# Optimization experiments

Hardware: AMD Instinct MI355X
Metric: run time of the kernel (lower is better)

## Reference

```python
import jax, jax.numpy as jnp
import numpy as np

MASK_VALUE = -1000000.0  # matches torch sequence_mask fill value


def setup_inputs() -> dict:
    key = jax.random.key(0)
    k1, k2, k3, k4 = jax.random.split(key, 4)
    B, Tq, Tk, d = 16, 2048, 2048, 128
    queries = jax.random.normal(k1, (B, Tq, d), dtype=jnp.float32)
    keys = jax.random.normal(k2, (B, Tk, d), dtype=jnp.float32)
    values = jax.random.normal(k3, (B, Tk, d), dtype=jnp.float32)
    valid_lens = jax.random.randint(k4, (B, Tq), 0, Tk, dtype=jnp.int64)
    return {"queries": queries, "keys": keys, "values": values,
            "valid_lens": valid_lens}


def reference(queries, keys, values, valid_lens):
    d = queries.shape[-1]
    Tk = keys.shape[1]
    # scores: [B, Tq, Tk]
    scores = jnp.einsum('bqd,bkd->bqk', queries, keys) / jnp.sqrt(
        jnp.asarray(d, dtype=queries.dtype))
    # per-row length mask: position k is valid iff k < valid_lens[b, q]
    mask = jnp.arange(Tk)[None, None, :] < valid_lens[:, :, None]
    scores = jnp.where(mask, scores, jnp.asarray(MASK_VALUE, scores.dtype))
    attn = jax.nn.softmax(scores, axis=-1)
    # dropout p=0.0 -> identity
    return jnp.einsum('bqk,bkd->bqd', attn, values)
```

## Files before the change

### kernel.cpp

```cpp
#include <hip/hip_runtime.h>
#include <stdint.h>
#include <math.h>

#define NB 16
#define TQ 2048
#define TK 2048
#define DH 128
#define KT (TK / 64)

#define QK_STR 136
#define VT_STR 72
#define P_STR  72

typedef __attribute__((ext_vector_type(8))) short bf16x8;
typedef __attribute__((ext_vector_type(4))) float f32x4;
typedef __attribute__((ext_vector_type(8))) unsigned short u16x8;

__device__ __forceinline__ unsigned short f2b(float f) {
  union { float f; uint32_t u; } v; v.f = f;
  uint32_t u = v.u;
  return (unsigned short)((u + 0x7fffu + ((u >> 16) & 1u)) >> 16);
}

__device__ __forceinline__ u16x8 cvt8(const float* p) {
  const f32x4 a = *(const f32x4*)p;
  const f32x4 b = *(const f32x4*)(p + 4);
  u16x8 o;
#pragma unroll
  for (int j = 0; j < 4; ++j) { o[j] = f2b(a[j]); o[4 + j] = f2b(b[j]); }
  return o;
}

__global__ __launch_bounds__(256) void prep_kernel(const float* __restrict__ K,
                                                   const float* __restrict__ V,
                                                   unsigned short* __restrict__ Kb,
                                                   unsigned short* __restrict__ Vt) {
  __shared__ alignas(16) unsigned short tile[64][136];
  const int t = threadIdx.x;
  const int b = blockIdx.y;
  const int kt = blockIdx.x;
  const int k0 = kt * 64;

  const float* Ks = K + ((size_t)b * TK + k0) * DH;
  unsigned short* Kd = Kb + ((size_t)b * TK + k0) * DH;
#pragma unroll
  for (int i = 0; i < 4; ++i) {
    const int row = i * 16 + (t >> 4);
    const int c0 = (t & 15) * 8;
    *(u16x8*)(Kd + (size_t)row * DH + c0) = cvt8(Ks + (size_t)row * DH + c0);
  }
  const float* Vs = V + ((size_t)b * TK + k0) * DH;
#pragma unroll
  for (int i = 0; i < 4; ++i) {
    const int row = i * 16 + (t >> 4);
    const int c0 = (t & 15) * 8;
    *(u16x8*)(&tile[row][c0]) = cvt8(Vs + (size_t)row * DH + c0);
  }
  __syncthreads();
  {
    const int d = t >> 1;
    const int half = t & 1;
    alignas(16) unsigned short tmp[32];
#pragma unroll
    for (int j = 0; j < 32; ++j) tmp[j] = tile[half * 32 + j][d];
    unsigned short* dst = Vt + ((size_t)(b * KT + kt) * DH + d) * 64 + half * 32;
#pragma unroll
    for (int j = 0; j < 4; ++j)
      *(u16x8*)(dst + j * 8) = *(const u16x8*)(&tmp[j * 8]);
  }
}

__global__ __launch_bounds__(256) void attn_ws(const float* __restrict__ Q,
                                               const unsigned short* __restrict__ Kp,
                                               const unsigned short* __restrict__ Vp,
                                               const int* __restrict__ vlen,
                                               float* __restrict__ out) {
  __shared__ alignas(16) char smem[53248];
  __shared__ int s_bvl[4];
  unsigned short* sQ = (unsigned short*)smem;
  unsigned short* sK = (unsigned short*)(smem + 17408);
  unsigned short* sV = (unsigned short*)(smem + 34816);

  const int tid  = threadIdx.x;
  const int w    = tid >> 6;
  const int lane = tid & 63;
  const int quad = lane >> 4;
  const int l15  = lane & 15;
  const int b    = blockIdx.y;
  const int q0   = blockIdx.x * 64;

  const float* Qb = Q + ((size_t)b * TQ + q0) * DH;
#pragma unroll
  for (int i = 0; i < 4; ++i) {
    const int row = i * 16 + (tid >> 4);
    const int c0 = (tid & 15) * 8;
    *(u16x8*)(sQ + row * QK_STR + c0) = cvt8(Qb + (size_t)row * DH + c0);
  }

  int hw = 0;
#pragma unroll
  for (int i = 0; i < 8; ++i) hw |= vlen[2 * i + 1];
  const bool is64 = (hw == 0);

  const float kScaleL2 = 0.08838834764831845f * 1.4426950408889634f;
  const float kBias    = -32.0f;
  const float kKill    = -1.0e7f;

  const int qw = q0 + w * 16;
  int vlr[4];
  float scl[4];
#pragma unroll
  for (int r = 0; r < 4; ++r) {
    const int idx = b * TQ + qw + quad * 4 + r;
    int v = is64 ? vlen[2 * idx] : vlen[idx];
    v = (v < 0) ? 0 : ((v > TK) ? TK : v);
    scl[r] = (v == 0) ? 0.0f : kScaleL2;
    vlr[r] = (v == 0) ? TK : v;
  }
  int wvl = 0;
#pragma unroll
  for (int r = 0; r < 4; ++r) wvl = max(wvl, vlr[r]);
  wvl = max(wvl, __shfl_xor(wvl, 16, 64));
  wvl = max(wvl, __shfl_xor(wvl, 32, 64));
  if (lane == 0) s_bvl[w] = wvl;

  __syncthreads();
  const int bvl = max(max(s_bvl[0], s_bvl[1]), max(s_bvl[2], s_bvl[3]));
  const int nt = (bvl + 63) >> 6;

  bf16x8 qa[4];
  {
    const unsigned short* qrow = sQ + (w * 16 + l15) * QK_STR;
#pragma unroll
    for (int kc = 0; kc < 4; ++kc)
      qa[kc] = *(const bf16x8*)(qrow + (kc * 4 + quad) * 8);
  }
  unsigned short* sP = (unsigned short*)smem + w * (16 * P_STR);

  f32x4 Of[8] = {};
  float l_r[4] = {0.f, 0.f, 0.f, 0.f};

  const unsigned short* Kbase = Kp + (size_t)b * TK * DH;
  const unsigned short* Vbase = Vp + (size_t)(b * KT) * DH * 64;
  const int krow = tid >> 4;
  const int kch  = tid & 15;

  u16x8 kreg[4], vreg[4];
  {
#pragma unroll
    for (int i = 0; i < 4; ++i)
      kreg[i] = *(const u16x8*)(Kbase + (size_t)(i * 16 + krow) * DH + kch * 8);
#pragma unroll
    for (int i = 0; i < 4; ++i)
      vreg[i] = *(const u16x8*)(Vbase + (i * 256 + tid) * 8);
  }

  for (int t = 0; t < nt; ++t) {
#pragma unroll
    for (int i = 0; i < 4; ++i)
      *(u16x8*)(sK + (i * 16 + krow) * QK_STR + kch * 8) = kreg[i];
#pragma unroll
    for (int i = 0; i < 4; ++i) {
      const int chunk = i * 256 + tid;
      *(u16x8*)(sV + (chunk >> 3) * VT_STR + (chunk & 7) * 8) = vreg[i];
    }
    __syncthreads();

    if (t + 1 < nt) {
      const unsigned short* Ksrc = Kbase + (size_t)(t + 1) * 64 * DH;
#pragma unroll
      for (int i = 0; i < 4; ++i)
        kreg[i] = *(const u16x8*)(Ksrc + (size_t)(i * 16 + krow) * DH + kch * 8);
      const unsigned short* Vsrc = Vbase + (size_t)(t + 1) * (DH * 64);
#pragma unroll
      for (int i = 0; i < 4; ++i)
        vreg[i] = *(const u16x8*)(Vsrc + (i * 256 + tid) * 8);
    }

    const int k0 = t * 64;
    if (k0 < wvl) {
      f32x4 sc[4] = {};
#pragma unroll
      for (int ct = 0; ct < 4; ++ct) {
        const unsigned short* kr = sK + (ct * 16 + l15) * QK_STR;
#pragma unroll
        for (int kc = 0; kc < 4; ++kc) {
          const bf16x8 kf = *(const bf16x8*)(kr + (kc * 4 + quad) * 8);
          sc[ct] = __builtin_amdgcn_mfma_f32_16x16x32_bf16(qa[kc], kf, sc[ct], 0, 0, 0);
        }
      }

      unsigned short pb[4][4];
#pragma unroll
      for (int ct = 0; ct < 4; ++ct) {
        const int kpos = k0 + ct * 16 + l15;
#pragma unroll
        for (int r = 0; r < 4; ++r) {
          const float s = (kpos < vlr[r]) ? fmaf(sc[ct][r], scl[r], kBias) : kKill;
          const float p = exp2f(s);
          l_r[r] += p;
          pb[ct][r] = f2b(p);
        }
      }

#pragma unroll
      for (int ct = 0; ct < 4; ++ct)
#pragma unroll
        for (int r = 0; r < 4; ++r)
          sP[(quad * 4 + r) * P_STR + ct * 16 + l15] = pb[ct][r];
      __asm__ __volatile__("" ::: "memory");

      bf16x8 pa[2];
      {
        const unsigned short* pr = sP + l15 * P_STR;
#pragma unroll
        for (int ch = 0; ch < 2; ++ch)
          pa[ch] = *(const bf16x8*)(pr + (ch * 4 + quad) * 8);
      }

#pragma unroll
      for (int dt = 0; dt < 8; ++dt) {
        const unsigned short* vr = sV + (dt * 16 + l15) * VT_STR;
#pragma unroll
        for (int ch = 0; ch < 2; ++ch) {
          const bf16x8 vf = *(const bf16x8*)(vr + (ch * 4 + quad) * 8);
          Of[dt] = __builtin_amdgcn_mfma_f32_16x16x32_bf16(pa[ch], vf, Of[dt], 0, 0, 0);
        }
      }
    }
    __syncthreads();
  }

#pragma unroll
  for (int off = 1; off <= 8; off <<= 1)
#pragma unroll
    for (int r = 0; r < 4; ++r)
      l_r[r] += __shfl_xor(l_r[r], off, 64);

#pragma unroll
  for (int r = 0; r < 4; ++r) {
    const float inv = 1.0f / l_r[r];
    const int q = qw + quad * 4 + r;
    float* orow = out + ((size_t)b * TQ + q) * DH;
#pragma unroll
    for (int dt = 0; dt < 8; ++dt)
      orow[dt * 16 + l15] = Of[dt][r] * inv;
  }
}

__global__ __launch_bounds__(256) void attn_fb(const float* __restrict__ Q,
                                               const float* __restrict__ Kp,
                                               const float* __restrict__ Vp,
                                               const int* __restrict__ vlen,
                                               float* __restrict__ out) {
  __shared__ alignas(16) char smem[53248];
  __shared__ int s_bvl[4];
  unsigned short* sQ = (unsigned short*)smem;
  unsigned short* sK = (unsigned short*)(smem + 17408);
  unsigned short* sV = (unsigned short*)(smem + 34816);

  const int tid  = threadIdx.x;
  const int w    = tid >> 6;
  const int lane = tid & 63;
  const int quad = lane >> 4;
  const int l15  = lane & 15;
  const int b    = blockIdx.y;
  const int q0   = blockIdx.x * 64;

  const float* Qb = Q + ((size_t)b * TQ + q0) * DH;
#pragma unroll
  for (int i = 0; i < 4; ++i) {
    const int row = i * 16 + (tid >> 4);
    const int c0 = (tid & 15) * 8;
    *(u16x8*)(sQ + row * QK_STR + c0) = cvt8(Qb + (size_t)row * DH + c0);
  }

  int hw = 0;
#pragma unroll
  for (int i = 0; i < 8; ++i) hw |= vlen[2 * i + 1];
  const bool is64 = (hw == 0);

  const float kScaleL2 = 0.08838834764831845f * 1.4426950408889634f;
  const float kBias    = -32.0f;
  const float kKill    = -1.0e7f;

  const int qw = q0 + w * 16;
  int vlr[4];
  float scl[4];
#pragma unroll
  for (int r = 0; r < 4; ++r) {
    const int idx = b * TQ + qw + quad * 4 + r;
    int v = is64 ? vlen[2 * idx] : vlen[idx];
    v = (v < 0) ? 0 : ((v > TK) ? TK : v);
    scl[r] = (v == 0) ? 0.0f : kScaleL2;
    vlr[r] = (v == 0) ? TK : v;
  }
  int wvl = 0;
#pragma unroll
  for (int r = 0; r < 4; ++r) wvl = max(wvl, vlr[r]);
  wvl = max(wvl, __shfl_xor(wvl, 16, 64));
  wvl = max(wvl, __shfl_xor(wvl, 32, 64));
  if (lane == 0) s_bvl[w] = wvl;
  __syncthreads();
  const int bvl = max(max(s_bvl[0], s_bvl[1]), max(s_bvl[2], s_bvl[3]));
  const int nt = (bvl + 63) >> 6;

  bf16x8 qa[4];
  {
    const unsigned short* qrow = sQ + (w * 16 + l15) * QK_STR;
#pragma unroll
    for (int kc = 0; kc < 4; ++kc)
      qa[kc] = *(const bf16x8*)(qrow + (kc * 4 + quad) * 8);
  }
  unsigned short* sP = (unsigned short*)smem + w * (16 * P_STR);

  f32x4 Of[8] = {};
  float l_r[4] = {0.f, 0.f, 0.f, 0.f};

  const float* Kb = Kp + (size_t)b * TK * DH;
  const float* Vb = Vp + (size_t)b * TK * DH;

  for (int t = 0; t < nt; ++t) {
    const int k0 = t * 64;
    __syncthreads();
#pragma unroll
    for (int i = 0; i < 4; ++i) {
      const int row = i * 16 + (tid >> 4);
      const int c0 = (tid & 15) * 8;
      *(u16x8*)(sK + row * QK_STR + c0) = cvt8(Kb + (size_t)(k0 + row) * DH + c0);
    }
#pragma unroll
    for (int i = 0; i < 4; ++i) {
      const int row = i * 16 + (tid >> 4);
      const int c0 = (tid & 15) * 8;
      *(u16x8*)(sV + row * QK_STR + c0) = cvt8(Vb + (size_t)(k0 + row) * DH + c0);
    }
    __syncthreads();
    if (k0 >= wvl) continue;

    f32x4 sc[4] = {};
#pragma unroll
    for (int ct = 0; ct < 4; ++ct) {
      const unsigned short* kr = sK + (ct * 16 + l15) * QK_STR;
#pragma unroll
      for (int kc = 0; kc < 4; ++kc) {
        const bf16x8 kf = *(const bf16x8*)(kr + (kc * 4 + quad) * 8);
        sc[ct] = __builtin_amdgcn_mfma_f32_16x16x32_bf16(qa[kc], kf, sc[ct], 0, 0, 0);
      }
    }
    unsigned short pb[4][4];
#pragma unroll
    for (int ct = 0; ct < 4; ++ct) {
      const int kpos = k0 + ct * 16 + l15;
#pragma unroll
      for (int r = 0; r < 4; ++r) {
        const float s = (kpos < vlr[r]) ? fmaf(sc[ct][r], scl[r], kBias) : kKill;
        const float p = exp2f(s);
        l_r[r] += p;
        pb[ct][r] = f2b(p);
      }
    }
#pragma unroll
    for (int ct = 0; ct < 4; ++ct)
#pragma unroll
      for (int r = 0; r < 4; ++r)
        sP[(quad * 4 + r) * P_STR + ct * 16 + l15] = pb[ct][r];
    __asm__ __volatile__("" ::: "memory");
    bf16x8 pa[2];
    {
      const unsigned short* pr = sP + l15 * P_STR;
#pragma unroll
      for (int ch = 0; ch < 2; ++ch)
        pa[ch] = *(const bf16x8*)(pr + (ch * 4 + quad) * 8);
    }
#pragma unroll
    for (int dt = 0; dt < 8; ++dt) {
      const int col = dt * 16 + l15;
#pragma unroll
      for (int ch = 0; ch < 2; ++ch) {
        bf16x8 vf;
#pragma unroll
        for (int j = 0; j < 8; ++j) {
          const int k = ch * 32 + quad * 8 + j;
          vf[j] = ((const short*)sV)[k * QK_STR + col];
        }
        Of[dt] = __builtin_amdgcn_mfma_f32_16x16x32_bf16(pa[ch], vf, Of[dt], 0, 0, 0);
      }
    }
  }

#pragma unroll
  for (int off = 1; off <= 8; off <<= 1)
#pragma unroll
    for (int r = 0; r < 4; ++r)
      l_r[r] += __shfl_xor(l_r[r], off, 64);

#pragma unroll
  for (int r = 0; r < 4; ++r) {
    const float inv = 1.0f / l_r[r];
    const int q = qw + quad * 4 + r;
    float* orow = out + ((size_t)b * TQ + q) * DH;
#pragma unroll
    for (int dt = 0; dt < 8; ++dt)
      orow[dt * 16 + l15] = Of[dt][r] * inv;
  }
}

extern "C" void kernel_launch(void* const* d_in, const int* in_sizes, int n_in,
                              void* d_out, int out_size, void* d_ws, size_t ws_size,
                              hipStream_t stream) {
  const float* Q = (const float*)d_in[0];
  const float* K = (const float*)d_in[1];
  const float* V = (const float*)d_in[2];
  const int* vl  = (const int*)d_in[3];
  float* out     = (float*)d_out;

  const size_t kb = (size_t)NB * TK * DH;
  if (ws_size >= kb * 2 * 2) {
    unsigned short* Kb = (unsigned short*)d_ws;
    unsigned short* Vt = Kb + kb;
    prep_kernel<<<dim3(KT, NB), 256, 0, stream>>>(K, V, Kb, Vt);
    attn_ws<<<dim3(TQ / 64, NB), 256, 0, stream>>>(Q, Kb, Vt, vl, out);
  } else {
    attn_fb<<<dim3(TQ / 64, NB), 256, 0, stream>>>(Q, K, V, vl, out);
  }
}
```

Before: 169.4 us.

## Sort queries by valid length and split key range across two blocks

Adds a per-batch counting sort that orders query rows by descending effective valid length, so each 64-row tile groups similar lengths and can stop scanning keys earlier. It also splits each tile's key loop into two halves run by separate blocks, writing unnormalised partial outputs and row sums that a new combine kernel adds, normalises and scatters back to original row order. The aim is to cut wasted masked key tiles and balance work across CUs. The cost is two extra launches, a workspace round trip for the partial outputs, and gathered Q loads.

```diff
diff --git a/kernel.cpp b/kernel.cpp
--- a/kernel.cpp
+++ b/kernel.cpp
@@ -7,6 +7,7 @@
 #define TK 2048
 #define DH 128
 #define KT (TK / 64)
+#define QB (TQ / 64)
 
 #define QK_STR 136
 #define VT_STR 72
@@ -29,6 +30,55 @@
 #pragma unroll
   for (int j = 0; j < 4; ++j) { o[j] = f2b(a[j]); o[4 + j] = f2b(b[j]); }
   return o;
+}
+
+__global__ __launch_bounds__(256) void sort_kernel(const int* __restrict__ vlen,
+                                                   int* __restrict__ perm) {
+  __shared__ int cnt[TK + 1];
+  __shared__ int base_[TK + 1];
+  __shared__ int psum[256];
+  const int b = blockIdx.x;
+  const int t = threadIdx.x;
+
+  int hw = 0;
+#pragma unroll
+  for (int i = 0; i < 8; ++i) hw |= vlen[2 * i + 1];
+  const bool is64 = (hw == 0);
+
+  for (int i = t; i <= TK; i += 256) cnt[i] = 0;
+  __syncthreads();
+
+  int eff[8];
+#pragma unroll
+  for (int j = 0; j < 8; ++j) {
+    const int q = j * 256 + t;
+    const int idx = b * TQ + q;
+    int v = is64 ? vlen[2 * idx] : vlen[idx];
+    v = (v < 0) ? 0 : ((v > TK) ? TK : v);
+    eff[j] = (v == 0) ? TK : v;
+    atomicAdd(&cnt[eff[j]], 1);
+  }
+  __syncthreads();
+
+  int loc[8]; int s = 0;
+#pragma unroll
+  for (int j = 0; j < 8; ++j) { loc[j] = cnt[TK - (t * 8 + j)]; s += loc[j]; }
+  psum[t] = s;
+  __syncthreads();
+  if (t == 0) {
+    int acc = 0;
+    for (int i = 0; i < 256; ++i) { const int x = psum[i]; psum[i] = acc; acc += x; }
+  }
+  __syncthreads();
+  int run = psum[t];
+#pragma unroll
+  for (int j = 0; j < 8; ++j) { base_[TK - (t * 8 + j)] = run; run += loc[j]; }
+  __syncthreads();
+#pragma unroll
+  for (int j = 0; j < 8; ++j) {
+    const int rank = atomicAdd(&base_[eff[j]], 1);
+    perm[b * TQ + rank] = j * 256 + t;
+  }
 }
 
 __global__ __launch_bounds__(256) void prep_kernel(const float* __restrict__ K,
@@ -74,7 +124,11 @@
                                                const unsigned short* __restrict__ Kp,
                                                const unsigned short* __restrict__ Vp,
                                                const int* __restrict__ vlen,
-                                               float* __restrict__ out) {
+                                               const int* __restrict__ perm,
+                                               float* __restrict__ pO,
+                                               float* __restrict__ pL,
+                                               float* __restrict__ out,
+                                               const int split) {
   __shared__ alignas(16) char smem[53248];
   __shared__ int s_bvl[4];
   unsigned short* sQ = (unsigned short*)smem;
@@ -87,14 +141,17 @@
   const int quad = lane >> 4;
   const int l15  = lane & 15;
   const int b    = blockIdx.y;
-  const int q0   = blockIdx.x * 64;
-
-  const float* Qb = Q + ((size_t)b * TQ + q0) * DH;
+  int jq, cchunk;
+  if (split) { jq = blockIdx.x >> 1; cchunk = blockIdx.x & 1; }
+  else       { jq = blockIdx.x;      cchunk = 0; }
+  const int q0 = jq * 64;
+
 #pragma unroll
   for (int i = 0; i < 4; ++i) {
     const int row = i * 16 + (tid >> 4);
+    const int qi = perm ? perm[b * TQ + q0 + row] : (q0 + row);
     const int c0 = (tid & 15) * 8;
-    *(u16x8*)(sQ + row * QK_STR + c0) = cvt8(Qb + (size_t)row * DH + c0);
+    *(u16x8*)(sQ + row * QK_STR + c0) = cvt8(Q + ((size_t)b * TQ + qi) * DH + c0);
   }
 
   int hw = 0;
@@ -109,9 +166,13 @@
   const int qw = q0 + w * 16;
   int vlr[4];
   float scl[4];
+  int qidx[4];
 #pragma unroll
   for (int r = 0; r < 4; ++r) {
-    const int idx = b * TQ + qw + quad * 4 + r;
+    const int rank = qw + quad * 4 + r;
+    const int qrow = perm ? perm[b * TQ + rank] : rank;
+    qidx[r] = qrow;
+    const int idx = b * TQ + qrow;
     int v = is64 ? vlen[2 * idx] : vlen[idx];
     v = (v < 0) ? 0 : ((v > TK) ? TK : v);
     scl[r] = (v == 0) ? 0.0f : kScaleL2;
@@ -127,6 +188,12 @@
   __syncthreads();
   const int bvl = max(max(s_bvl[0], s_bvl[1]), max(s_bvl[2], s_bvl[3]));
   const int nt = (bvl + 63) >> 6;
+  int t0 = 0, t1 = nt;
+  if (split) {
+    const int half = (nt + 1) >> 1;
+    t0 = cchunk * half;
+    t1 = cchunk ? nt : half;
+  }
 
   bf16x8 qa[4];
   {
@@ -146,16 +213,18 @@
   const int kch  = tid & 15;
 
   u16x8 kreg[4], vreg[4];
-  {
+  if (t0 < t1) {
+    const unsigned short* Ksrc = Kbase + (size_t)t0 * 64 * DH;
 #pragma unroll
     for (int i = 0; i < 4; ++i)
-      kreg[i] = *(const u16x8*)(Kbase + (size_t)(i * 16 + krow) * DH + kch * 8);
+      kreg[i] = *(const u16x8*)(Ksrc + (size_t)(i * 16 + krow) * DH + kch * 8);
+    const unsigned short* Vsrc = Vbase + (size_t)t0 * (DH * 64);
 #pragma unroll
     for (int i = 0; i < 4; ++i)
-      vreg[i] = *(const u16x8*)(Vbase + (i * 256 + tid) * 8);
-  }
-
-  for (int t = 0; t < nt; ++t) {
+      vreg[i] = *(const u16x8*)(Vsrc + (i * 256 + tid) * 8);
+  }
+
+  for (int t = t0; t < t1; ++t) {
 #pragma unroll
     for (int i = 0; i < 4; ++i)
       *(u16x8*)(sK + (i * 16 + krow) * QK_STR + kch * 8) = kreg[i];
@@ -166,7 +235,7 @@
     }
     __syncthreads();
 
-    if (t + 1 < nt) {
+    if (t + 1 < t1) {
       const unsigned short* Ksrc = Kbase + (size_t)(t + 1) * 64 * DH;
 #pragma unroll
       for (int i = 0; i < 4; ++i)
@@ -237,14 +306,56 @@
     for (int r = 0; r < 4; ++r)
       l_r[r] += __shfl_xor(l_r[r], off, 64);
 
-#pragma unroll
-  for (int r = 0; r < 4; ++r) {
-    const float inv = 1.0f / l_r[r];
-    const int q = qw + quad * 4 + r;
-    float* orow = out + ((size_t)b * TQ + q) * DH;
-#pragma unroll
-    for (int dt = 0; dt < 8; ++dt)
-      orow[dt * 16 + l15] = Of[dt][r] * inv;
+  if (split) {
+    const int slot = (b * QB + jq) * 2 + cchunk;
+    float* po = pO + (size_t)slot * (64 * DH);
+    float* pl = pL + (size_t)slot * 64;
+#pragma unroll
+    for (int r = 0; r < 4; ++r) {
+      const int row = w * 16 + quad * 4 + r;
+#pragma unroll
+      for (int dt = 0; dt < 8; ++dt)
+        po[(size_t)row * DH + dt * 16 + l15] = Of[dt][r];
+    }
+    if (l15 == 0) {
+#pragma unroll
+      for (int r = 0; r < 4; ++r)
+        pl[w * 16 + quad * 4 + r] = l_r[r];
+    }
+  } else {
+#pragma unroll
+    for (int r = 0; r < 4; ++r) {
+      const float inv = 1.0f / l_r[r];
+      float* orow = out + ((size_t)b * TQ + qidx[r]) * DH;
+#pragma unroll
+      for (int dt = 0; dt < 8; ++dt)
+        orow[dt * 16 + l15] = Of[dt][r] * inv;
+    }
+  }
+}
+
+__global__ __launch_bounds__(256) void combine_kernel(const float* __restrict__ pO,
+                                                      const float* __restrict__ pL,
+                                                      const int* __restrict__ perm,
+                                                      float* __restrict__ out) {
+  const int b = blockIdx.y;
+  const int j = blockIdx.x;
+  const int t = threadIdx.x;
+  const int s0 = (b * QB + j) * 2;
+  const float* a0 = pO + (size_t)s0 * (64 * DH);
+  const float* a1 = a0 + 64 * DH;
+  const float* l0 = pL + (size_t)s0 * 64;
+#pragma unroll
+  for (int i = 0; i < 8; ++i) {
+    const int u = i * 256 + t;
+    const int r = u >> 5;
+    const int d4 = (u & 31) * 4;
+    const float l = l0[r] + l0[64 + r];
+    const float inv = 1.0f / l;
+    const f32x4 x = *(const f32x4*)(a0 + (size_t)r * DH + d4);
+    const f32x4 y = *(const f32x4*)(a1 + (size_t)r * DH + d4);
+    const int qi = perm[b * TQ + j * 64 + r];
+    *(f32x4*)(out + ((size_t)b * TQ + qi) * DH + d4) = (x + y) * inv;
   }
 }
 
@@ -415,13 +526,35 @@
   const int* vl  = (const int*)d_in[3];
   float* out     = (float*)d_out;
 
-  const size_t kb = (size_t)NB * TK * DH;
-  if (ws_size >= kb * 2 * 2) {
+  const size_t kb    = (size_t)NB * TK * DH;
+  const size_t kvB   = kb * 2 * 2;
+  const size_t permB = (size_t)NB * TQ * sizeof(int);
+  const size_t pLB   = (size_t)NB * QB * 2 * 64 * sizeof(float);
+  const size_t pOB   = (size_t)NB * QB * 2 * 64 * DH * sizeof(float);
+
+  if (ws_size >= kvB + permB + pLB + pOB) {
+    unsigned short* Kb = (unsigned short*)d_ws;
+    unsigned short* Vt = Kb + kb;
+    int*   perm = (int*)((char*)d_ws + kvB);
+    float* pL   = (float*)((char*)d_ws + kvB + permB);
+    float* pO   = (float*)((char*)d_ws + kvB + permB + pLB);
+    sort_kernel<<<dim3(NB), 256, 0, stream>>>(vl, perm);
+    prep_kernel<<<dim3(KT, NB), 256, 0, stream>>>(K, V, Kb, Vt);
+    attn_ws<<<dim3(QB * 2, NB), 256, 0, stream>>>(Q, Kb, Vt, vl, perm, pO, pL, out, 1);
+    combine_kernel<<<dim3(QB, NB), 256, 0, stream>>>(pO, pL, perm, out);
+  } else if (ws_size >= kvB + permB) {
+    unsigned short* Kb = (unsigned short*)d_ws;
+    unsigned short* Vt = Kb + kb;
+    int* perm = (int*)((char*)d_ws + kvB);
+    sort_kernel<<<dim3(NB), 256, 0, stream>>>(vl, perm);
+    prep_kernel<<<dim3(KT, NB), 256, 0, stream>>>(K, V, Kb, Vt);
+    attn_ws<<<dim3(QB, NB), 256, 0, stream>>>(Q, Kb, Vt, vl, perm, nullptr, nullptr, out, 0);
+  } else if (ws_size >= kvB) {
     unsigned short* Kb = (unsigned short*)d_ws;
     unsigned short* Vt = Kb + kb;
     prep_kernel<<<dim3(KT, NB), 256, 0, stream>>>(K, V, Kb, Vt);
-    attn_ws<<<dim3(TQ / 64, NB), 256, 0, stream>>>(Q, Kb, Vt, vl, out);
+    attn_ws<<<dim3(QB, NB), 256, 0, stream>>>(Q, Kb, Vt, vl, nullptr, nullptr, nullptr, out, 0);
   } else {
-    attn_fb<<<dim3(TQ / 64, NB), 256, 0, stream>>>(Q, K, V, vl, out);
-  }
-}
+    attn_fb<<<dim3(QB, NB), 256, 0, stream>>>(Q, K, V, vl, out);
+  }
+}
```

Measured after the change: 189.0 us. +11.6%, slower.
